# Performance work log

Measured on AMD Instinct MI355X. Metric: run time of the kernel, lower is better.

## Reference

```python
import jax, jax.numpy as jnp
import numpy as np

B, S, E = 2, 2048, 1024
H = 1344            # hidden_dim = ceil(1.3*1024/64)*64
NH = 4              # mLSTM heads
DH = H // NH        # 336
K = 4               # causal conv kernel size
NPH = H // 4        # headwise proj heads (qkv_proj_blocksize=4)
PD = H // NPH       # per-head proj dim = 4
EPS = 1e-6


def setup_inputs() -> dict:
    key = jax.random.key(0)
    ks = jax.random.split(key, 10)
    s_in = jnp.sqrt(2.0 / (5 * E))    # small_init(E)
    s_pd = jnp.sqrt(2.0 / (5 * PD))   # small_init per-head dim
    return {
        "x": jax.random.normal(ks[0], (B, S, E), jnp.float32),
        "W_up": jax.random.normal(ks[1], (E, 2 * H), jnp.float32) * s_in,
        "conv_k": jax.random.normal(ks[2], (K, 1, H), jnp.float32) * jnp.sqrt(2.0 / K),  # depthwise, WIO layout
        "conv_b": jnp.zeros((H,), jnp.float32),
        "Wq": jax.random.normal(ks[3], (NPH, PD, PD), jnp.float32) * s_pd,
        "Wk": jax.random.normal(ks[4], (NPH, PD, PD), jnp.float32) * s_pd,
        "Wv": jax.random.normal(ks[5], (NPH, PD, PD), jnp.float32) * s_pd,
        "W_ig": jax.random.normal(ks[6], (3 * H, NH), jnp.float32) * 0.01,
        "b_ig": jax.random.normal(ks[7], (NH,), jnp.float32) * 0.1,
        "W_fg": jax.random.normal(ks[8], (3 * H, NH), jnp.float32) * 0.01,
        "b_fg": jnp.linspace(3.0, 6.0, NH, dtype=jnp.float32),
        "ln_w": jnp.ones((H,), jnp.float32),
        "skip": jnp.ones((H,), jnp.float32),
        "W_down": jax.random.normal(ks[9], (H, E), jnp.float32) * (2.0 / 12 / np.sqrt(H)),
    }


def _headwise(x, W):
    # LinearHeadwiseExpand: block-diagonal projection over NPH heads of size PD
    xh = x.reshape(B, S, NPH, PD)
    return jnp.einsum('bshd,hdo->bsho', xh, W).reshape(B, S, H)


def _mlstm_cell(q, k, v, ig, fg):
    # parallel stabilized mLSTM; q,k,v: (B,NH,S,DH); ig,fg: (B,NH,S)
    logf = jax.nn.log_sigmoid(fg)
    c = jnp.cumsum(logf, axis=-1)                         # (B,NH,S)
    logfmat = c[..., :, None] - c[..., None, :]           # (B,NH,S,S) cumulative forget decay
    mask = jnp.tril(jnp.ones((S, S), bool))               # causal mask
    log_D = jnp.where(mask, logfmat, -jnp.inf) + ig[..., None, :]
    m = jnp.max(log_D, axis=-1, keepdims=True)            # rowwise stabilizer
    D = jnp.exp(log_D - m)
    qk = jnp.einsum('bnsd,bntd->bnst', q, k) * (DH ** -0.5)
    C = qk * D
    n = jnp.maximum(jnp.abs(jnp.sum(C, axis=-1, keepdims=True)), jnp.exp(-m))
    return jnp.einsum('bnst,bntd->bnsd', C / (n + EPS), v)


def reference(x, W_up, conv_k, conv_b, Wq, Wk, Wv, W_ig, b_ig, W_fg, b_fg, ln_w, skip, W_down):
    x_inner = x @ W_up                                    # (B,S,2H)
    x_m, z = jnp.split(x_inner, 2, axis=-1)
    # depthwise causal conv1d
    xp = jnp.pad(x_m, ((0, 0), (K - 1, 0), (0, 0)))
    xc = jax.lax.conv_general_dilated(
        xp, conv_k, (1,), 'VALID',
        dimension_numbers=('NWC', 'WIO', 'NWC'),
        feature_group_count=H) + conv_b
    act = jax.nn.silu(xc)
    q = _headwise(act, Wq)
    k = _headwise(act, Wk)
    v = _headwise(x_m, Wv)
    gin = jnp.concatenate([q, k, v], axis=-1)             # (B,S,3H)
    ig = jnp.transpose(gin @ W_ig + b_ig, (0, 2, 1))      # (B,NH,S)
    fg = jnp.transpose(gin @ W_fg + b_fg, (0, 2, 1))
    qh = jnp.transpose(q.reshape(B, S, NH, DH), (0, 2, 1, 3))
    kh = jnp.transpose(k.reshape(B, S, NH, DH), (0, 2, 1, 3))
    vh = jnp.transpose(v.reshape(B, S, NH, DH), (0, 2, 1, 3))
    h = _mlstm_cell(qh, kh, vh, ig, fg)                   # (B,NH,S,DH)
    # multi-head layernorm (per-head groupnorm over DH, scale only)
    mu = jnp.mean(h, axis=-1, keepdims=True)
    var = jnp.var(h, axis=-1, keepdims=True)
    hn = (h - mu) * jax.lax.rsqrt(var + 1e-5) * ln_w.reshape(NH, 1, DH)
    h_out = jnp.transpose(hn, (0, 2, 1, 3)).reshape(B, S, H)
    h_state = (h_out + skip * act) * jax.nn.silu(z)
    return h_state @ W_down
```

## Files before the change

kernel.cpp:

```cpp
#include <hip/hip_runtime.h>
#include <cmath>

#define DI __device__ __forceinline__

constexpr int B_=2, S_=2048, E_=1024, H_=1344, NH_=4, DH_=336;
constexpr int BS_=B_*S_, H2_=2*H_;
constexpr int NG_=B_*NH_*S_;

constexpr size_t N_X=(size_t)BS_*E_;
constexpr size_t N_WUP=(size_t)E_*H2_;
constexpr size_t N_WDN=(size_t)H_*E_;
constexpr size_t N_BSH=(size_t)BS_*H_;
constexpr size_t N_BSH2=(size_t)BS_*H2_;
constexpr size_t N_WH=5376, N_WG=16128, N_CK=4*H_;

constexpr size_t O_IGB = 64;
constexpr size_t O_LOGF= O_IGB + NG_;
constexpr size_t O_AB  = O_LOGF+ NG_;
constexpr size_t O_MB  = O_AB  + NG_;
constexpr size_t O_MTB = O_MB  + NG_;
constexpr size_t O_CK  = O_MTB + NG_;
constexpr size_t O_CB  = O_CK  + N_CK;
constexpr size_t O_WQ  = O_CB  + H_;
constexpr size_t O_WK  = O_WQ  + N_WH;
constexpr size_t O_WV  = O_WK  + N_WH;
constexpr size_t O_WIG = O_WV  + N_WH;
constexpr size_t O_BIG = O_WIG + N_WG;
constexpr size_t O_WFG = O_BIG + 16;
constexpr size_t O_BFG = O_WFG + N_WG;
constexpr size_t O_LNW = O_BFG + 16;
constexpr size_t O_SKP = O_LNW + H_;
constexpr size_t O_FX  = O_SKP + H_;
constexpr size_t O_FWUP= O_FX  + N_X;
constexpr size_t O_FWDN= O_FWUP+ N_WUP;
constexpr size_t O_XIN = O_FWDN+ N_WDN;
constexpr size_t O_ACT = O_XIN + N_BSH2;
constexpr size_t O_QB  = O_ACT + N_BSH;
constexpr size_t O_KB  = O_QB  + N_BSH;
constexpr size_t O_VB  = O_KB  + N_BSH;
constexpr size_t O_HOUT= O_VB  + N_BSH;

constexpr size_t KSPLIT_SHORTS=(size_t)8*128*11*64*8;
constexpr size_t VT_SHORTS=(size_t)8*64*22*64*8;

typedef __attribute__((ext_vector_type(8))) short bf16x8;
typedef __attribute__((ext_vector_type(4))) float f32x4;

DI float bf2f(unsigned int u){union{unsigned int i;float f;}v;v.i=(u&0xffffu)<<16;return v.f;}
DI unsigned short f2bf(float f){union{float f;unsigned int i;}v;v.f=f;unsigned int x=v.i;
  return (unsigned short)((x+0x7fffu+((x>>16)&1u))>>16);}
DI float siluf(float x){return x/(1.f+expf(-x));}
DI float logsigf(float x){return (x>=0.f)?-log1pf(expf(-x)):x-log1pf(expf(x));}
DI void load4(const float* p, float* d){float4 v=*reinterpret_cast<const float4*>(p);
  d[0]=v.x;d[1]=v.y;d[2]=v.z;d[3]=v.w;}

__global__ __launch_bounds__(256) void detect_k(const unsigned short* __restrict__ xraw,
                                                int* __restrict__ flag){
  __shared__ int cnt_s;
  if(threadIdx.x==0) cnt_s=0;
  __syncthreads();
  int c=0;
  for(int i=threadIdx.x;i<2048;i+=256){
    const unsigned e=(xraw[i]>>7)&0xFFu;
    if(e>=0x90u) c++;
  }
  atomicAdd(&cnt_s,c);
  __syncthreads();
  if(threadIdx.x==0) *flag=(cnt_s>16)?0:1;
}

constexpr int CV0=5376, CV1=CV0+1344, CV2=CV1+5376, CV3=CV2+5376, CV4=CV3+5376,
              CV5=CV4+16128, CV6=CV5+4, CV7=CV6+16128, CV8=CV7+4,
              CV9=CV8+1344, CVT=CV9+1344;
__global__ __launch_bounds__(256) void convall_k(
    const void* s0,const void* s1,const void* s2,const void* s3,const void* s4,
    const void* s5,const void* s6,const void* s7,const void* s8,const void* s9,
    const void* s10, float* __restrict__ ws, const int* __restrict__ flag){
  const int i=blockIdx.x*256+threadIdx.x;
  if(i>=CVT) return;
  const void* src; int off; size_t dst;
  if(i<CV0){src=s0; off=i;      dst=O_CK +off;}
  else if(i<CV1){src=s1; off=i-CV0; dst=O_CB +off;}
  else if(i<CV2){src=s2; off=i-CV1; dst=O_WQ +off;}
  else if(i<CV3){src=s3; off=i-CV2; dst=O_WK +off;}
  else if(i<CV4){src=s4; off=i-CV3; dst=O_WV +off;}
  else if(i<CV5){src=s5; off=i-CV4; dst=O_WIG+off;}
  else if(i<CV6){src=s6; off=i-CV5; dst=O_BIG+off;}
  else if(i<CV7){src=s7; off=i-CV6; dst=O_WFG+off;}
  else if(i<CV8){src=s8; off=i-CV7; dst=O_BFG+off;}
  else if(i<CV9){src=s9; off=i-CV8; dst=O_LNW+off;}
  else          {src=s10;off=i-CV9; dst=O_SKP+off;}
  ws[dst]=(*flag)?bf2f(((const unsigned short*)src)[off])
                 :((const float*)src)[off];
}

__global__ __launch_bounds__(256) void aprep_k(const void* __restrict__ src,
                                               const int* __restrict__ flag,
                                               int kcn,int ldk,int total,
                                               unsigned short* __restrict__ hi,
                                               unsigned short* __restrict__ lo){
  const int slot=blockIdx.x*256+threadIdx.x;
  if(slot>=total) return;
  const int l=slot&63, rest=slot>>6;
  const int kc=rest%kcn, mt=rest/kcn;
  const int row=mt*16+(l&15), k0=kc*32+(l>>4)*8;
  const int fl=flag?*flag:0;
  float v[8];
  if(fl){
    const unsigned short* s=(const unsigned short*)src+(size_t)row*ldk+k0;
    const uint4 u=*reinterpret_cast<const uint4*>(s);
    v[0]=bf2f(u.x);v[1]=bf2f(u.x>>16);v[2]=bf2f(u.y);v[3]=bf2f(u.y>>16);
    v[4]=bf2f(u.z);v[5]=bf2f(u.z>>16);v[6]=bf2f(u.w);v[7]=bf2f(u.w>>16);
  }else{
    const float* s=(const float*)src+(size_t)row*ldk+k0;
    load4(s,v); load4(s+4,v+4);
  }
  unsigned short h8[8], l8[8];
#pragma unroll
  for(int j=0;j<8;j++){ h8[j]=f2bf(v[j]); l8[j]=f2bf(v[j]-bf2f(h8[j])); }
  uint4 ph,pl;
  ph.x=(unsigned)h8[0]|((unsigned)h8[1]<<16); ph.y=(unsigned)h8[2]|((unsigned)h8[3]<<16);
  ph.z=(unsigned)h8[4]|((unsigned)h8[5]<<16); ph.w=(unsigned)h8[6]|((unsigned)h8[7]<<16);
  pl.x=(unsigned)l8[0]|((unsigned)l8[1]<<16); pl.y=(unsigned)l8[2]|((unsigned)l8[3]<<16);
  pl.z=(unsigned)l8[4]|((unsigned)l8[5]<<16); pl.w=(unsigned)l8[6]|((unsigned)l8[7]<<16);
  *reinterpret_cast<uint4*>(&hi[(size_t)slot*8])=ph;
  *reinterpret_cast<uint4*>(&lo[(size_t)slot*8])=pl;
}

__global__ __launch_bounds__(256) void bprep_k(const void* __restrict__ src,
                                               const int* __restrict__ flag,
                                               int kcn,int ldn,int total,
                                               unsigned short* __restrict__ hi,
                                               unsigned short* __restrict__ lo){
  const int slot=blockIdx.x*256+threadIdx.x;
  if(slot>=total) return;
  const int l=slot&63, rest=slot>>6;
  const int kc=rest%kcn, nt=rest/kcn;
  const int col=nt*16+(l&15), row0=kc*32+(l>>4)*8;
  const int fl=flag?*flag:0;
  float v[8];
  if(fl){
    const unsigned short* s=(const unsigned short*)src;
#pragma unroll
    for(int j=0;j<8;j++) v[j]=bf2f(s[(size_t)(row0+j)*ldn+col]);
  }else{
    const float* s=(const float*)src;
#pragma unroll
    for(int j=0;j<8;j++) v[j]=s[(size_t)(row0+j)*ldn+col];
  }
  unsigned short h8[8], l8[8];
#pragma unroll
  for(int j=0;j<8;j++){ h8[j]=f2bf(v[j]); l8[j]=f2bf(v[j]-bf2f(h8[j])); }
  uint4 ph,pl;
  ph.x=(unsigned)h8[0]|((unsigned)h8[1]<<16); ph.y=(unsigned)h8[2]|((unsigned)h8[3]<<16);
  ph.z=(unsigned)h8[4]|((unsigned)h8[5]<<16); ph.w=(unsigned)h8[6]|((unsigned)h8[7]<<16);
  pl.x=(unsigned)l8[0]|((unsigned)l8[1]<<16); pl.y=(unsigned)l8[2]|((unsigned)l8[3]<<16);
  pl.z=(unsigned)l8[4]|((unsigned)l8[5]<<16); pl.w=(unsigned)l8[6]|((unsigned)l8[7]<<16);
  *reinterpret_cast<uint4*>(&hi[(size_t)slot*8])=ph;
  *reinterpret_cast<uint4*>(&lo[(size_t)slot*8])=pl;
}

__global__ __launch_bounds__(256) void gemm2_k(
    const unsigned short* __restrict__ Ahi, const unsigned short* __restrict__ Alo,
    const unsigned short* __restrict__ Bhi, const unsigned short* __restrict__ Blo,
    void* __restrict__ C, const int* __restrict__ flag, int kcn, int ldc){
  const int t=threadIdx.x, w=t>>6, l=t&63, lm=l&15, quad=l>>4;
  const int bn=blockIdx.x*128, bm=blockIdx.y*128;
  const int mtg0=bm>>4, ntg0=bn>>4;

  __shared__ short TT[2][32*512];

  f32x4 acc[2][8];
#pragma unroll
  for(int g=0;g<2;g++)
#pragma unroll
    for(int nt=0;nt<8;nt++) acc[g][nt]={0.f,0.f,0.f,0.f};

  auto stage=[&](int buf,int kc){
#pragma unroll
    for(int j=0;j<8;j++){
      const int tr=w*8+j;
      const unsigned short* src;
      if(tr<8)       src=&Ahi[((size_t)(mtg0+tr   )*kcn+kc)*512+(size_t)l*8];
      else if(tr<16) src=&Alo[((size_t)(mtg0+tr-8 )*kcn+kc)*512+(size_t)l*8];
      else if(tr<24) src=&Bhi[((size_t)(ntg0+tr-16)*kcn+kc)*512+(size_t)l*8];
      else           src=&Blo[((size_t)(ntg0+tr-24)*kcn+kc)*512+(size_t)l*8];
      __builtin_amdgcn_global_load_lds(
        (const __attribute__((address_space(1))) unsigned int*)src,
        (__attribute__((address_space(3))) unsigned int*)&TT[buf][tr*512],
        16,0,0);
    }
  };

  auto compute=[&](int buf){
    const short* Tb=&TT[buf][0];
    const bf16x8 ah0=*reinterpret_cast<const bf16x8*>(&Tb[(2*w  )*512+l*8]);
    const bf16x8 ah1=*reinterpret_cast<const bf16x8*>(&Tb[(2*w+1)*512+l*8]);
    const bf16x8 al0=*reinterpret_cast<const bf16x8*>(&Tb[(8+2*w  )*512+l*8]);
    const bf16x8 al1=*reinterpret_cast<const bf16x8*>(&Tb[(8+2*w+1)*512+l*8]);
#pragma unroll
    for(int nt=0;nt<8;nt++){
      const bf16x8 bh=*reinterpret_cast<const bf16x8*>(&Tb[(16+nt)*512+l*8]);
      const bf16x8 bl=*reinterpret_cast<const bf16x8*>(&Tb[(24+nt)*512+l*8]);
      acc[0][nt]=__builtin_amdgcn_mfma_f32_16x16x32_bf16(ah0,bh,acc[0][nt],0,0,0);
      acc[0][nt]=__builtin_amdgcn_mfma_f32_16x16x32_bf16(al0,bh,acc[0][nt],0,0,0);
      acc[0][nt]=__builtin_amdgcn_mfma_f32_16x16x32_bf16(ah0,bl,acc[0][nt],0,0,0);
      acc[1][nt]=__builtin_amdgcn_mfma_f32_16x16x32_bf16(ah1,bh,acc[1][nt],0,0,0);
      acc[1][nt]=__builtin_amdgcn_mfma_f32_16x16x32_bf16(al1,bh,acc[1][nt],0,0,0);
      acc[1][nt]=__builtin_amdgcn_mfma_f32_16x16x32_bf16(ah1,bl,acc[1][nt],0,0,0);
    }
  };

  stage(0,0);
  __syncthreads();
  for(int kc=0;kc<kcn;kc++){
    const int cur=kc&1;
    if(kc+1<kcn) stage(cur^1,kc+1);
    compute(cur);
    __syncthreads();
  }

  const int bf=flag?*flag:0;
#pragma unroll
  for(int g=0;g<2;g++)
#pragma unroll
    for(int nt=0;nt<8;nt++)
#pragma unroll
      for(int r=0;r<4;r++){
        const size_t idx=(size_t)(bm+(2*w+g)*16+quad*4+r)*ldc+bn+nt*16+lm;
        if(bf) ((unsigned short*)C)[idx]=f2bf(acc[g][nt][r]);
        else   ((float*)C)[idx]=acc[g][nt][r];
      }
}

__global__ __launch_bounds__(256) void conv_act_k(const float* __restrict__ xin,
                                                  const float* __restrict__ ck,
                                                  const float* __restrict__ cb,
                                                  float* __restrict__ act){
  const int i=blockIdx.x*256+threadIdx.x;
  if(i>=(int)N_BSH) return;
  const int bs=i/H_, h=i-bs*H_;
  const int b=bs/S_, s=bs-b*S_;
  float xc=cb[h];
#pragma unroll
  for(int w=0;w<4;w++){
    const int sr=s-3+w;
    if(sr>=0) xc+=xin[(size_t)(b*S_+sr)*H2_+h]*ck[w*H_+h];
  }
  act[(size_t)bs*H_+h]=siluf(xc);
}

__global__ __launch_bounds__(256) void qkv_k(const float* __restrict__ act,
                                             const float* __restrict__ xin,
                                             const float* __restrict__ Wq,
                                             const float* __restrict__ Wk,
                                             const float* __restrict__ Wv,
                                             float* __restrict__ qb,float* __restrict__ kb,
                                             float* __restrict__ vb){
  const int i=blockIdx.x*256+threadIdx.x;
  if(i>=(int)N_BSH) return;
  const int bs=i/H_, h=i-bs*H_;
  const int b=bs/S_, s=bs-b*S_;
  const int ph=h>>2, o=h&3, base=ph*4;
  float q=0.f,k=0.f,v=0.f;
#pragma unroll
  for(int d=0;d<4;d++){
    const float a=act[(size_t)bs*H_+base+d];
    const float x=xin[(size_t)bs*H2_+base+d];
    q+=a*Wq[ph*16+d*4+o];
    k+=a*Wk[ph*16+d*4+o];
    v+=x*Wv[ph*16+d*4+o];
  }
  const int nh=h/DH_, dh=h-nh*DH_;
  const size_t off=((size_t)(b*NH_+nh)*S_+s)*DH_+dh;
  qb[off]=q; kb[off]=k; vb[off]=v;
}

__global__ __launch_bounds__(256) void gates2_k(const float* __restrict__ qb,
                                                const float* __restrict__ kb,
                                                const float* __restrict__ vb,
                                                const float* __restrict__ Wig,
                                                const float* __restrict__ big,
                                                const float* __restrict__ Wfg,
                                                const float* __restrict__ bfg,
                                                float* __restrict__ igb,
                                                float* __restrict__ logfb){
  const int wid=(blockIdx.x*256+threadIdx.x)>>6;
  const int l=threadIdx.x&63;
  if(wid>=BS_) return;
  const int b=wid>>11, s=wid&2047;
  float aI0=0.f,aI1=0.f,aI2=0.f,aI3=0.f;
  float aF0=0.f,aF1=0.f,aF2=0.f,aF3=0.f;
  for(int nh=0;nh<NH_;nh++){
    const size_t rb=((size_t)(b*NH_+nh)*S_+s)*DH_;
    const int hb=nh*DH_;
    for(int dh=l;dh<DH_;dh+=64){
      const int h=hb+dh;
      const float q=qb[rb+dh], k=kb[rb+dh], v=vb[rb+dh];
      const float4 wiq=*reinterpret_cast<const float4*>(&Wig[(size_t)h*4]);
      const float4 wik=*reinterpret_cast<const float4*>(&Wig[(size_t)(H_+h)*4]);
      const float4 wiv=*reinterpret_cast<const float4*>(&Wig[(size_t)(2*H_+h)*4]);
      const float4 wfq=*reinterpret_cast<const float4*>(&Wfg[(size_t)h*4]);
      const float4 wfk=*reinterpret_cast<const float4*>(&Wfg[(size_t)(H_+h)*4]);
      const float4 wfv=*reinterpret_cast<const float4*>(&Wfg[(size_t)(2*H_+h)*4]);
      aI0+=q*wiq.x+k*wik.x+v*wiv.x;
      aI1+=q*wiq.y+k*wik.y+v*wiv.y;
      aI2+=q*wiq.z+k*wik.z+v*wiv.z;
      aI3+=q*wiq.w+k*wik.w+v*wiv.w;
      aF0+=q*wfq.x+k*wfk.x+v*wfv.x;
      aF1+=q*wfq.y+k*wfk.y+v*wfv.y;
      aF2+=q*wfq.z+k*wfk.z+v*wfv.z;
      aF3+=q*wfq.w+k*wfk.w+v*wfv.w;
    }
  }
#pragma unroll
  for(int m=1;m<64;m<<=1){
    aI0+=__shfl_xor(aI0,m); aI1+=__shfl_xor(aI1,m);
    aI2+=__shfl_xor(aI2,m); aI3+=__shfl_xor(aI3,m);
    aF0+=__shfl_xor(aF0,m); aF1+=__shfl_xor(aF1,m);
    aF2+=__shfl_xor(aF2,m); aF3+=__shfl_xor(aF3,m);
  }
  if(l==0){
    const size_t o0=(size_t)(b*NH_+0)*S_+s;
    const size_t o1=(size_t)(b*NH_+1)*S_+s;
    const size_t o2=(size_t)(b*NH_+2)*S_+s;
    const size_t o3=(size_t)(b*NH_+3)*S_+s;
    igb[o0]=aI0+big[0]; igb[o1]=aI1+big[1];
    igb[o2]=aI2+big[2]; igb[o3]=aI3+big[3];
    logfb[o0]=logsigf(aF0+bfg[0]); logfb[o1]=logsigf(aF1+bfg[1]);
    logfb[o2]=logsigf(aF2+bfg[2]); logfb[o3]=logsigf(aF3+bfg[3]);
  }
}

__global__ __launch_bounds__(256) void kprep_k(const float* __restrict__ kb,
                                               unsigned short* __restrict__ khi,
                                               unsigned short* __restrict__ klo){
  const int blk=blockIdx.x;
  const int head=blk>>7, tt=blk&127;
  const size_t obase=(size_t)blk*11*512;
  for(int slot=threadIdx.x; slot<704; slot+=256){
    const int dc=slot>>6, ll=slot&63, quad=ll>>4, lm=ll&15;
    const int tg=tt*16+lm, dbase=dc*32+quad*8;
    float v[8];
    if(dbase<336){
      load4(&kb[((size_t)head*S_+tg)*DH_+dbase],v);
      load4(&kb[((size_t)head*S_+tg)*DH_+dbase+4],v+4);
    } else { for(int j=0;j<8;j++) v[j]=0.f; }
    unsigned short hi8[8], lo8[8];
#pragma unroll
    for(int j=0;j<8;j++){
      hi8[j]=f2bf(v[j]);
      lo8[j]=f2bf(v[j]-bf2f(hi8[j]));
    }
    const size_t o=obase+(size_t)(dc*64+ll)*8;
    uint4 ph, pl;
    ph.x=(unsigned)hi8[0]|((unsigned)hi8[1]<<16); ph.y=(unsigned)hi8[2]|((unsigned)hi8[3]<<16);
    ph.z=(unsigned)hi8[4]|((unsigned)hi8[5]<<16); ph.w=(unsigned)hi8[6]|((unsigned)hi8[7]<<16);
    pl.x=(unsigned)lo8[0]|((unsigned)lo8[1]<<16); pl.y=(unsigned)lo8[2]|((unsigned)lo8[3]<<16);
    pl.z=(unsigned)lo8[4]|((unsigned)lo8[5]<<16); pl.w=(unsigned)lo8[6]|((unsigned)lo8[7]<<16);
    *reinterpret_cast<uint4*>(&khi[o])=ph;
    *reinterpret_cast<uint4*>(&klo[o])=pl;
  }
}

__global__ __launch_bounds__(256) void vprep_k(const float* __restrict__ vb,
                                               unsigned short* __restrict__ vTf){
  const int blk=blockIdx.x;
  const int head=blk>>6, tc=blk&63;
  const size_t obase=(size_t)blk*22*512;
  for(int slot=threadIdx.x; slot<1408; slot+=256){
    const int ntg=slot>>6, ll=slot&63, quad=ll>>4, lm=ll&15;
    const int n=ntg*16+lm, t0=tc*32+quad*8;
    unsigned short h8[8];
#pragma unroll
    for(int j=0;j<8;j++){
      float val;
      if(n<336)       val=vb[((size_t)head*S_+t0+j)*DH_+n];
      else if(n==336) val=1.f;
      else            val=0.f;
      h8[j]=f2bf(val);
    }
    uint4 pk;
    pk.x=(unsigned)h8[0]|((unsigned)h8[1]<<16); pk.y=(unsigned)h8[2]|((unsigned)h8[3]<<16);
    pk.z=(unsigned)h8[4]|((unsigned)h8[5]<<16); pk.w=(unsigned)h8[6]|((unsigned)h8[7]<<16);
    *reinterpret_cast<uint4*>(&vTf[obase+(size_t)(ntg*64+ll)*8])=pk;
  }
}

__global__ __launch_bounds__(256) void scan_k(const float* __restrict__ igb,
                                              const float* __restrict__ logfb,
                                              float* __restrict__ ab,float* __restrict__ Mb,
                                              float* __restrict__ mtb){
  const int head=blockIdx.x, t=threadIdx.x;
  __shared__ float sh[256];
  const float* lf=logfb+(size_t)head*S_;
  const float* ig=igb+(size_t)head*S_;
  float lc[8];
  float run=0.f;
#pragma unroll
  for(int i=0;i<8;i++){ run+=lf[t*8+i]; lc[i]=run; }
  sh[t]=run;
  for(int st=1;st<256;st<<=1){
    __syncthreads();
    const float v=(t>=st)?sh[t-st]:0.f;
    __syncthreads();
    sh[t]+=v;
  }
  __syncthreads();
  const float off=(t==0)?0.f:sh[t-1];
  __syncthreads();
  float av[8],mv[8],cv[8];
  float mrun=-1e30f;
#pragma unroll
  for(int i=0;i<8;i++){
    cv[i]=off+lc[i];
    av[i]=ig[t*8+i]-cv[i];
    mrun=fmaxf(mrun,av[i]);
    mv[i]=mrun;
  }
  sh[t]=mrun;
  for(int st=1;st<256;st<<=1){
    __syncthreads();
    const float v=(t>=st)?sh[t-st]:-1e30f;
    __syncthreads();
    sh[t]=fmaxf(sh[t],v);
  }
  __syncthreads();
  const float moff=(t==0)?-1e30f:sh[t-1];
#pragma unroll
  for(int i=0;i<8;i++){
    const float Mi=fmaxf(moff,mv[i]);
    const size_t j=(size_t)head*S_+t*8+i;
    ab[j]=av[i]; Mb[j]=Mi; mtb[j]=cv[i]+Mi;
  }
}

__global__ __launch_bounds__(512,1) void mlstm6_k(
    const float* __restrict__ qb, const unsigned short* __restrict__ khi,
    const unsigned short* __restrict__ klo, const unsigned short* __restrict__ vTf,
    const float* __restrict__ ab, const float* __restrict__ Mb,
    float* __restrict__ part, float* __restrict__ rsum){
  const int bid=blockIdx.x;
  const int head=bid&7;
  const int rest=bid>>3;
  const int pairI=rest&7, seg=rest>>3;
  const int t=threadIdx.x, w=t>>6, l=t&63, lm=l&15, quad=l>>4;

  __shared__ short KV[2][66*512];
  __shared__ short Sc[8][16][40];

  const size_t hb=(size_t)head*S_;
  const float scale=0.05455447256f;

  const int sbA=pairI, sbB=15-pairI;
  const int nA=pairI+1, nTot=17;

  bf16x8 qh[11], ql[11];
  f32x4 accO[22];
  float Mr[4];
  int ws0=sbA*128+w*16;

  auto loadQ=[&](int ws0_){
    const float* qrow=qb+(hb+ws0_+lm)*DH_;
#pragma unroll
    for(int dc=0;dc<11;dc++){
      const int dbase=dc*32+quad*8;
      float v[8];
      if(dbase<336){ load4(qrow+dbase,v); load4(qrow+dbase+4,v+4); }
      else { for(int j=0;j<8;j++) v[j]=0.f; }
#pragma unroll
      for(int j=0;j<8;j++){
        const unsigned short h=f2bf(v[j]);
        qh[dc][j]=(short)h;
        ql[dc][j]=(short)f2bf(v[j]-bf2f(h));
      }
    }
#pragma unroll
    for(int r=0;r<4;r++) Mr[r]=Mb[hb+ws0_+quad*4+r];
#pragma unroll
    for(int n=0;n<22;n++) accO[n]={0.f,0.f,0.f,0.f};
  };

  auto itemC=[&](int i)->int{
    return (i<nA)? (seg+4*i) : (seg+4*(i-nA));
  };

  auto stage=[&](int buf,int c){
    const size_t kbase=(((size_t)head*128+(size_t)(2*c))*11)*512+(size_t)l*8;
    const size_t vbase=(((size_t)head*64+(size_t)c)*22)*512+(size_t)l*8;
#pragma unroll
    for(int j=0;j<9;j++){
      const int tr=w+8*j;
      if(tr<66){
        const unsigned short* src;
        if(tr<22)      src=&khi[kbase+(size_t)tr*512];
        else if(tr<44) src=&klo[kbase+(size_t)(tr-22)*512];
        else           src=&vTf[vbase+(size_t)(tr-44)*512];
        __builtin_amdgcn_global_load_lds(
          (const __attribute__((address_space(1))) unsigned int*)src,
          (__attribute__((address_space(3))) unsigned int*)&KV[buf][(size_t)tr*512],
          16,0,0);
      }
    }
  };

  auto compute=[&](int c,int buf){
    const int t0=c<<5;
    if(t0>ws0+15) return;
    const float al0=ab[hb+t0+lm];
    const float al1=ab[hb+t0+16+lm];
#pragma unroll
    for(int tt=0;tt<2;tt++){
      f32x4 a0={0,0,0,0}, a1={0,0,0,0}, a2={0,0,0,0};
#pragma unroll
      for(int dc=0;dc<11;dc++){
        const bf16x8 kh=*reinterpret_cast<const bf16x8*>(&KV[buf][(tt*11+dc)*512+l*8]);
        const bf16x8 kl=*reinterpret_cast<const bf16x8*>(&KV[buf][(22+tt*11+dc)*512+l*8]);
        a0=__builtin_amdgcn_mfma_f32_16x16x32_bf16(qh[dc],kh,a0,0,0,0);
        a1=__builtin_amdgcn_mfma_f32_16x16x32_bf16(ql[dc],kh,a1,0,0,0);
        a2=__builtin_amdgcn_mfma_f32_16x16x32_bf16(qh[dc],kl,a2,0,0,0);
      }
      const float al=(tt==0)?al0:al1;
      const int tg=t0+tt*16+lm;
#pragma unroll
      for(int r=0;r<4;r++){
        const int srow=quad*4+r;
        const float qk=a0[r]+a1[r]+a2[r];
        const float e=fminf(al-Mr[r],0.f);
        const float msk=(tg<=ws0+srow)?1.f:0.f;
        Sc[w][srow][tt*16+lm]=(short)f2bf(msk*(qk*scale*expf(e)));
      }
    }
    const bf16x8 scf=*reinterpret_cast<const bf16x8*>(&Sc[w][lm][quad*8]);
#pragma unroll
    for(int nt=0;nt<22;nt++){
      const bf16x8 vf=*reinterpret_cast<const bf16x8*>(&KV[buf][(44+nt)*512+l*8]);
      accO[nt]=__builtin_amdgcn_mfma_f32_16x16x32_bf16(scf,vf,accO[nt],0,0,0);
    }
  };

  auto epilogue=[&](){
    const size_t pbase=(size_t)head*2048+ws0;
#pragma unroll
    for(int nt=0;nt<22;nt++){
      const int col=nt*16+lm;
#pragma unroll
      for(int r=0;r<4;r++){
        const int srow=quad*4+r;
        const float val=accO[nt][r];
        if(col<336){ if(val!=0.f) atomicAdd(&part[(pbase+srow)*336+col],val); }
        else if(col==336){ if(val!=0.f) atomicAdd(&rsum[pbase+srow],val); }
      }
    }
  };

  loadQ(ws0);
  stage(0,itemC(0));
  __syncthreads();
  int cur=0;
  for(int i=0;i<nTot;i++){
    if(i+1<nTot) stage(cur^1,itemC(i+1));
    compute(itemC(i),cur);
    if(i==nA-1){
      epilogue();
      ws0=sbB*128+w*16;
      loadQ(ws0);
    }
    __syncthreads();
    cur^=1;
  }
  epilogue();
}

__global__ __launch_bounds__(256) void finalize_k(const float* __restrict__ part,
                                                  const float* __restrict__ rsum,
                                                  const float* __restrict__ mtb,
                                                  const float* __restrict__ lnw,
                                                  float* __restrict__ hout){
  const int sblk=blockIdx.x, head=blockIdx.y;
  const int bI=head>>2, nh=head&3;
  const int s0=sblk*32;
  const int t=threadIdx.x, row=t>>3, sub=t&7;
  __shared__ float red1[32][8], red2[32][8];
  __shared__ float mu_s[32], rs_s[32], inv_s[32];
  const size_t pbase=(size_t)head*2048+s0;
  const float* prow=part+(pbase+row)*336;
  float s1=0.f,s2=0.f;
  for(int c=sub;c<336;c+=8){ const float v=prow[c]; s1+=v; s2+=v*v; }
  red1[row][sub]=s1; red2[row][sub]=s2;
  __syncthreads();
  if(sub==0){
    float a1=0.f,a2=0.f;
#pragma unroll
    for(int j=0;j<8;j++){ a1+=red1[row][j]; a2+=red2[row][j]; }
    const float mt=mtb[(size_t)head*S_+s0+row];
    const float nn=fmaxf(fabsf(rsum[pbase+row]), expf(fminf(fmaxf(-mt,-60.f),60.f)));
    const float inv=1.f/(nn+1e-6f);
    const float mu=a1*inv/336.f;
    const float var=a2*inv*inv/336.f-mu*mu;
    inv_s[row]=inv; mu_s[row]=mu;
    rs_s[row]=rsqrtf(fmaxf(var,0.f)+1e-5f);
  }
  __syncthreads();
  const float inv=inv_s[row], mu=mu_s[row], rs=rs_s[row];
  float* orow=hout+((size_t)(bI*S_+s0+row))*H_+nh*DH_;
  for(int c=sub;c<336;c+=8)
    orow[c]=(prow[c]*inv-mu)*rs*lnw[nh*DH_+c];
}

__global__ __launch_bounds__(256) void hstate_k(const float* __restrict__ hout,
                                                const float* __restrict__ act,
                                                const float* __restrict__ xin,
                                                const float* __restrict__ skip,
                                                float* __restrict__ hs){
  const int i=blockIdx.x*256+threadIdx.x;
  if(i>=(int)N_BSH) return;
  const int bs=i/H_, h=i-bs*H_;
  const float z=xin[(size_t)bs*H2_+H_+h];
  hs[(size_t)bs*H_+h]=(hout[(size_t)bs*H_+h]+skip[h]*act[(size_t)bs*H_+h])*siluf(z);
}

extern "C" void kernel_launch(void* const* d_in, const int* in_sizes, int n_in,
                              void* d_out, int out_size, void* d_ws, size_t ws_size,
                              hipStream_t stream){
  float* ws=(float*)d_ws;
  int* flag=(int*)ws;

  float* igb  = ws+O_IGB;
  float* logfb= ws+O_LOGF;
  float* ab   = ws+O_AB;
  float* Mbuf = ws+O_MB;
  float* mtb  = ws+O_MTB;
  float* f_ck = ws+O_CK;
  float* f_cb = ws+O_CB;
  float* f_wq = ws+O_WQ;
  float* f_wk = ws+O_WK;
  float* f_wv = ws+O_WV;
  float* f_wig= ws+O_WIG;
  float* f_big= ws+O_BIG;
  float* f_wfg= ws+O_WFG;
  float* f_bfg= ws+O_BFG;
  float* f_lnw= ws+O_LNW;
  float* f_skp= ws+O_SKP;
  float* xin  = ws+O_XIN;
  float* act  = ws+O_ACT;
  float* qb   = ws+O_QB;
  float* kb   = ws+O_KB;
  float* vb   = ws+O_VB;
  float* hout = ws+O_HOUT;
  float* hs   = qb;

  unsigned short* xhi  =(unsigned short*)(ws+O_FX);   unsigned short* xlo  =xhi+N_X;
  unsigned short* wuphi=(unsigned short*)(ws+O_FWUP); unsigned short* wuplo=wuphi+N_WUP;
  unsigned short* wdnhi=(unsigned short*)(ws+O_FWDN); unsigned short* wdnlo=wdnhi+N_WDN;
  unsigned short* khi=(unsigned short*)(ws+O_FX);
  unsigned short* klo=khi+KSPLIT_SHORTS;
  unsigned short* vTf=(unsigned short*)kb;
  unsigned short* hshi=(unsigned short*)kb;
  unsigned short* hslo=hshi+N_BSH;
  float* partb=vb;
  float* rsumb=igb;

  detect_k<<<1,256,0,stream>>>((const unsigned short*)d_in[0],flag);
  convall_k<<<(CVT+255)/256,256,0,stream>>>(d_in[2],d_in[3],d_in[4],d_in[5],d_in[6],
                                            d_in[7],d_in[8],d_in[9],d_in[10],d_in[11],
                                            d_in[12],ws,flag);

  aprep_k<<<(256*32*64+255)/256,256,0,stream>>>(d_in[0],flag,32,1024,256*32*64,xhi,xlo);
  bprep_k<<<(168*32*64+255)/256,256,0,stream>>>(d_in[1],flag,32,2688,168*32*64,wuphi,wuplo);
  gemm2_k<<<dim3(2688/128,4096/128),256,0,stream>>>(xhi,xlo,wuphi,wuplo,xin,nullptr,32,H2_);

  conv_act_k<<<(int)((N_BSH+255)/256),256,0,stream>>>(xin,f_ck,f_cb,act);
  qkv_k<<<(int)((N_BSH+255)/256),256,0,stream>>>(act,xin,f_wq,f_wk,f_wv,qb,kb,vb);
  gates2_k<<<(BS_*64+255)/256,256,0,stream>>>(qb,kb,vb,f_wig,f_big,f_wfg,f_bfg,igb,logfb);
  kprep_k<<<8*128,256,0,stream>>>(kb,khi,klo);
  vprep_k<<<8*64,256,0,stream>>>(vb,vTf);
  bprep_k<<<(64*42*64+255)/256,256,0,stream>>>(d_in[13],flag,42,1024,64*42*64,wdnhi,wdnlo);
  scan_k<<<B_*NH_,256,0,stream>>>(igb,logfb,ab,Mbuf,mtb);
  hipMemsetAsync(partb,0,N_BSH*sizeof(float),stream);
  hipMemsetAsync(rsumb,0,(size_t)NG_*sizeof(float),stream);
  mlstm6_k<<<256,512,0,stream>>>(qb,khi,klo,vTf,ab,Mbuf,partb,rsumb);
  finalize_k<<<dim3(S_/32,B_*NH_),256,0,stream>>>(partb,rsumb,mtb,f_lnw,hout);
  hstate_k<<<(int)((N_BSH+255)/256),256,0,stream>>>(hout,act,xin,f_skp,hs);
  aprep_k<<<(256*42*64+255)/256,256,0,stream>>>(hs,nullptr,42,1344,256*42*64,hshi,hslo);
  gemm2_k<<<dim3(1024/128,4096/128),256,0,stream>>>(hshi,hslo,wdnhi,wdnlo,d_out,flag,42,E_);
}
```

Baseline: 503.4 us.

## Split mLSTM into smaller single-buffered blocks and fuse finalize with hstate

The mLSTM kernel now launches 1024 blocks of 256 threads, each handling one 64-row query block and one of four interleaved key-chunk segments. This replaces 256 blocks of 512 threads that paired short and long query blocks and double-buffered the key/value tiles. The aim is more blocks per CU and finer load balance, at the cost of losing the overlap between loading and compute, having more blocks with uneven work, and issuing more atomics. The finalize kernel now also applies the skip connection and the SiLU gate, removing the separate hstate pass and the hout buffer round trip.

```diff
diff --git a/kernel.cpp b/kernel.cpp
--- a/kernel.cpp
+++ b/kernel.cpp
@@ -435,33 +435,34 @@
   }
 }
 
-__global__ __launch_bounds__(512,1) void mlstm6_k(
+__global__ __launch_bounds__(256,2) void mlstm7_k(
     const float* __restrict__ qb, const unsigned short* __restrict__ khi,
     const unsigned short* __restrict__ klo, const unsigned short* __restrict__ vTf,
     const float* __restrict__ ab, const float* __restrict__ Mb,
     float* __restrict__ part, float* __restrict__ rsum){
   const int bid=blockIdx.x;
   const int head=bid&7;
-  const int rest=bid>>3;
-  const int pairI=rest&7, seg=rest>>3;
+  const int r=bid>>3;
+  const int seg=r&3;
+  const int sb=31-(r>>2);
+  const int cmax=2*sb+1;
+  const int nTot=(cmax>=seg)?((cmax-seg)>>2)+1:0;
+  if(nTot==0) return;
   const int t=threadIdx.x, w=t>>6, l=t&63, lm=l&15, quad=l>>4;
-
-  __shared__ short KV[2][66*512];
-  __shared__ short Sc[8][16][40];
+  const int ws0=sb*64+w*16;
+
+  __shared__ short KV[66*512];
+  __shared__ short Sc[4][16][40];
 
   const size_t hb=(size_t)head*S_;
   const float scale=0.05455447256f;
-
-  const int sbA=pairI, sbB=15-pairI;
-  const int nA=pairI+1, nTot=17;
 
   bf16x8 qh[11], ql[11];
   f32x4 accO[22];
   float Mr[4];
-  int ws0=sbA*128+w*16;
-
-  auto loadQ=[&](int ws0_){
-    const float* qrow=qb+(hb+ws0_+lm)*DH_;
+
+  {
+    const float* qrow=qb+(hb+ws0+lm)*DH_;
 #pragma unroll
     for(int dc=0;dc<11;dc++){
       const int dbase=dc*32+quad*8;
@@ -476,21 +477,17 @@
       }
     }
 #pragma unroll
-    for(int r=0;r<4;r++) Mr[r]=Mb[hb+ws0_+quad*4+r];
+    for(int rr=0;rr<4;rr++) Mr[rr]=Mb[hb+ws0+quad*4+rr];
 #pragma unroll
     for(int n=0;n<22;n++) accO[n]={0.f,0.f,0.f,0.f};
-  };
-
-  auto itemC=[&](int i)->int{
-    return (i<nA)? (seg+4*i) : (seg+4*(i-nA));
-  };
-
-  auto stage=[&](int buf,int c){
+  }
+
+  auto stage=[&](int c){
     const size_t kbase=(((size_t)head*128+(size_t)(2*c))*11)*512+(size_t)l*8;
     const size_t vbase=(((size_t)head*64+(size_t)c)*22)*512+(size_t)l*8;
 #pragma unroll
-    for(int j=0;j<9;j++){
-      const int tr=w+8*j;
+    for(int j=0;j<17;j++){
+      const int tr=w+4*j;
       if(tr<66){
         const unsigned short* src;
         if(tr<22)      src=&khi[kbase+(size_t)tr*512];
@@ -498,13 +495,13 @@
         else           src=&vTf[vbase+(size_t)(tr-44)*512];
         __builtin_amdgcn_global_load_lds(
           (const __attribute__((address_space(1))) unsigned int*)src,
-          (__attribute__((address_space(3))) unsigned int*)&KV[buf][(size_t)tr*512],
+          (__attribute__((address_space(3))) unsigned int*)&KV[(size_t)tr*512],
           16,0,0);
       }
     }
   };
 
-  auto compute=[&](int c,int buf){
+  auto compute=[&](int c){
     const int t0=c<<5;
     if(t0>ws0+15) return;
     const float al0=ab[hb+t0+lm];
@@ -514,8 +511,8 @@
       f32x4 a0={0,0,0,0}, a1={0,0,0,0}, a2={0,0,0,0};
 #pragma unroll
       for(int dc=0;dc<11;dc++){
-        const bf16x8 kh=*reinterpret_cast<const bf16x8*>(&KV[buf][(tt*11+dc)*512+l*8]);
-        const bf16x8 kl=*reinterpret_cast<const bf16x8*>(&KV[buf][(22+tt*11+dc)*512+l*8]);
+        const bf16x8 kh=*reinterpret_cast<const bf16x8*>(&KV[(tt*11+dc)*512+l*8]);
+        const bf16x8 kl=*reinterpret_cast<const bf16x8*>(&KV[(22+tt*11+dc)*512+l*8]);
         a0=__builtin_amdgcn_mfma_f32_16x16x32_bf16(qh[dc],kh,a0,0,0,0);
         a1=__builtin_amdgcn_mfma_f32_16x16x32_bf16(ql[dc],kh,a1,0,0,0);
         a2=__builtin_amdgcn_mfma_f32_16x16x32_bf16(qh[dc],kl,a2,0,0,0);
@@ -523,10 +520,10 @@
       const float al=(tt==0)?al0:al1;
       const int tg=t0+tt*16+lm;
 #pragma unroll
-      for(int r=0;r<4;r++){
-        const int srow=quad*4+r;
-        const float qk=a0[r]+a1[r]+a2[r];
-        const float e=fminf(al-Mr[r],0.f);
+      for(int rr=0;rr<4;rr++){
+        const int srow=quad*4+rr;
+        const float qk=a0[rr]+a1[rr]+a2[rr];
+        const float e=fminf(al-Mr[rr],0.f);
         const float msk=(tg<=ws0+srow)?1.f:0.f;
         Sc[w][srow][tt*16+lm]=(short)f2bf(msk*(qk*scale*expf(e)));
       }
@@ -534,49 +531,41 @@
     const bf16x8 scf=*reinterpret_cast<const bf16x8*>(&Sc[w][lm][quad*8]);
 #pragma unroll
     for(int nt=0;nt<22;nt++){
-      const bf16x8 vf=*reinterpret_cast<const bf16x8*>(&KV[buf][(44+nt)*512+l*8]);
+      const bf16x8 vf=*reinterpret_cast<const bf16x8*>(&KV[(44+nt)*512+l*8]);
       accO[nt]=__builtin_amdgcn_mfma_f32_16x16x32_bf16(scf,vf,accO[nt],0,0,0);
     }
   };
 
-  auto epilogue=[&](){
-    const size_t pbase=(size_t)head*2048+ws0;
-#pragma unroll
-    for(int nt=0;nt<22;nt++){
-      const int col=nt*16+lm;
-#pragma unroll
-      for(int r=0;r<4;r++){
-        const int srow=quad*4+r;
-        const float val=accO[nt][r];
-        if(col<336){ if(val!=0.f) atomicAdd(&part[(pbase+srow)*336+col],val); }
-        else if(col==336){ if(val!=0.f) atomicAdd(&rsum[pbase+srow],val); }
-      }
-    }
-  };
-
-  loadQ(ws0);
-  stage(0,itemC(0));
-  __syncthreads();
-  int cur=0;
   for(int i=0;i<nTot;i++){
-    if(i+1<nTot) stage(cur^1,itemC(i+1));
-    compute(itemC(i),cur);
-    if(i==nA-1){
-      epilogue();
-      ws0=sbB*128+w*16;
-      loadQ(ws0);
-    }
+    const int c=seg+4*i;
+    stage(c);
     __syncthreads();
-    cur^=1;
-  }
-  epilogue();
-}
-
-__global__ __launch_bounds__(256) void finalize_k(const float* __restrict__ part,
-                                                  const float* __restrict__ rsum,
-                                                  const float* __restrict__ mtb,
-                                                  const float* __restrict__ lnw,
-                                                  float* __restrict__ hout){
+    compute(c);
+    __syncthreads();
+  }
+
+  const size_t pbase=(size_t)head*2048+ws0;
+#pragma unroll
+  for(int nt=0;nt<22;nt++){
+    const int col=nt*16+lm;
+#pragma unroll
+    for(int rr=0;rr<4;rr++){
+      const int srow=quad*4+rr;
+      const float val=accO[nt][rr];
+      if(col<336){ if(val!=0.f) atomicAdd(&part[(pbase+srow)*336+col],val); }
+      else if(col==336){ if(val!=0.f) atomicAdd(&rsum[pbase+srow],val); }
+    }
+  }
+}
+
+__global__ __launch_bounds__(256) void finalize2_k(const float* __restrict__ part,
+                                                   const float* __restrict__ rsum,
+                                                   const float* __restrict__ mtb,
+                                                   const float* __restrict__ lnw,
+                                                   const float* __restrict__ skip,
+                                                   const float* __restrict__ act,
+                                                   const float* __restrict__ xin,
+                                                   float* __restrict__ hs){
   const int sblk=blockIdx.x, head=blockIdx.y;
   const int bI=head>>2, nh=head&3;
   const int s0=sblk*32;
@@ -603,21 +592,16 @@
   }
   __syncthreads();
   const float inv=inv_s[row], mu=mu_s[row], rs=rs_s[row];
-  float* orow=hout+((size_t)(bI*S_+s0+row))*H_+nh*DH_;
-  for(int c=sub;c<336;c+=8)
-    orow[c]=(prow[c]*inv-mu)*rs*lnw[nh*DH_+c];
-}
-
-__global__ __launch_bounds__(256) void hstate_k(const float* __restrict__ hout,
-                                                const float* __restrict__ act,
-                                                const float* __restrict__ xin,
-                                                const float* __restrict__ skip,
-                                                float* __restrict__ hs){
-  const int i=blockIdx.x*256+threadIdx.x;
-  if(i>=(int)N_BSH) return;
-  const int bs=i/H_, h=i-bs*H_;
-  const float z=xin[(size_t)bs*H2_+H_+h];
-  hs[(size_t)bs*H_+h]=(hout[(size_t)bs*H_+h]+skip[h]*act[(size_t)bs*H_+h])*siluf(z);
+  const size_t bsrow=(size_t)(bI*S_+s0+row);
+  float* orow=hs+bsrow*H_+nh*DH_;
+  const float* arow=act+bsrow*H_+nh*DH_;
+  const float* zrow=xin+bsrow*H2_+H_+nh*DH_;
+  const float* srw=skip+nh*DH_;
+  const float* lrw=lnw+nh*DH_;
+  for(int c=sub;c<336;c+=8){
+    const float hn=(prow[c]*inv-mu)*rs*lrw[c];
+    orow[c]=(hn+srw[c]*arow[c])*siluf(zrow[c]);
+  }
 }
 
 extern "C" void kernel_launch(void* const* d_in, const int* in_sizes, int n_in,
@@ -647,8 +631,6 @@
   float* qb   = ws+O_QB;
   float* kb   = ws+O_KB;
   float* vb   = ws+O_VB;
-  float* hout = ws+O_HOUT;
-  float* hs   = qb;
 
   unsigned short* xhi  =(unsigned short*)(ws+O_FX);   unsigned short* xlo  =xhi+N_X;
   unsigned short* wuphi=(unsigned short*)(ws+O_FWUP); unsigned short* wuplo=wuphi+N_WUP;
@@ -660,6 +642,7 @@
   unsigned short* hslo=hshi+N_BSH;
   float* partb=vb;
   float* rsumb=igb;
+  float* hs   = qb;
 
   detect_k<<<1,256,0,stream>>>((const unsigned short*)d_in[0],flag);
   convall_k<<<(CVT+255)/256,256,0,stream>>>(d_in[2],d_in[3],d_in[4],d_in[5],d_in[6],
@@ -679,9 +662,8 @@
   scan_k<<<B_*NH_,256,0,stream>>>(igb,logfb,ab,Mbuf,mtb);
   hipMemsetAsync(partb,0,N_BSH*sizeof(float),stream);
   hipMemsetAsync(rsumb,0,(size_t)NG_*sizeof(float),stream);
-  mlstm6_k<<<256,512,0,stream>>>(qb,khi,klo,vTf,ab,Mbuf,partb,rsumb);
-  finalize_k<<<dim3(S_/32,B_*NH_),256,0,stream>>>(partb,rsumb,mtb,f_lnw,hout);
-  hstate_k<<<(int)((N_BSH+255)/256),256,0,stream>>>(hout,act,xin,f_skp,hs);
+  mlstm7_k<<<1024,256,0,stream>>>(qb,khi,klo,vTf,ab,Mbuf,partb,rsumb);
+  finalize2_k<<<dim3(S_/32,B_*NH_),256,0,stream>>>(partb,rsumb,mtb,f_lnw,f_skp,act,xin,hs);
   aprep_k<<<(256*42*64+255)/256,256,0,stream>>>(hs,nullptr,42,1344,256*42*64,hshi,hslo);
   gemm2_k<<<dim3(1024/128,4096/128),256,0,stream>>>(hshi,hslo,wdnhi,wdnlo,d_out,flag,42,E_);
 }
```

Result: slower. 518.9 us (+3.1%).
